# Kernel tuning notes

Measured on AMD Instinct MI355X. Metric: run time of the kernel, lower is better.

## Reference

```python
import jax, jax.numpy as jnp
import numpy as np

HIDDEN = 2048
N_HEADS = 32
N_KV_HEADS = 8
HEAD_DIM = HIDDEN // N_HEADS  # 64
N_GROUPS = N_HEADS // N_KV_HEADS  # 4
EPS = 1e-6
BATCH = 2
SEQ = 2048


def setup_inputs() -> dict:
    key = jax.random.key(0)
    ks = jax.random.split(key, 8)
    s = 1.0 / np.sqrt(HIDDEN)
    return {
        "hidden_states": jax.random.normal(ks[0], (BATCH, SEQ, HIDDEN), jnp.float32),
        # torch nn.Linear weights: [out_features, in_features]
        "Wq": jax.random.normal(ks[1], (N_HEADS * HEAD_DIM, HIDDEN), jnp.float32) * s,
        "Wk": jax.random.normal(ks[2], (N_KV_HEADS * HEAD_DIM, HIDDEN), jnp.float32) * s,
        "Wv": jax.random.normal(ks[3], (N_KV_HEADS * HEAD_DIM, HIDDEN), jnp.float32) * s,
        "Wo": jax.random.normal(ks[4], (HIDDEN, N_HEADS * HEAD_DIM), jnp.float32) * s,
        "q_norm_weight": jnp.ones((HEAD_DIM,), jnp.float32),
        "k_norm_weight": jnp.ones((HEAD_DIM,), jnp.float32),
    }


def _rmsnorm(x, w, eps=EPS):
    # x: [..., head_dim]
    rms = jax.lax.rsqrt(jnp.mean(x * x, axis=-1, keepdims=True) + eps)
    return x * rms * w


def reference(hidden_states, Wq, Wk, Wv, Wo, q_norm_weight, k_norm_weight):
    B, S, _ = hidden_states.shape
    # projections (y = x @ W.T)
    q = jnp.einsum('bsh,oh->bso', hidden_states, Wq)
    k = jnp.einsum('bsh,oh->bso', hidden_states, Wk)
    v = jnp.einsum('bsh,oh->bso', hidden_states, Wv)
    # [B, H, S, D]
    q = q.reshape(B, S, N_HEADS, HEAD_DIM).transpose(0, 2, 1, 3)
    k = k.reshape(B, S, N_KV_HEADS, HEAD_DIM).transpose(0, 2, 1, 3)
    v = v.reshape(B, S, N_KV_HEADS, HEAD_DIM).transpose(0, 2, 1, 3)
    # GQA repeat_interleave along head dim
    k = jnp.repeat(k, N_GROUPS, axis=1)
    v = jnp.repeat(v, N_GROUPS, axis=1)
    # fused QK RMSNorm
    q = _rmsnorm(q, q_norm_weight)
    k = _rmsnorm(k, k_norm_weight)
    # scaled dot-product attention with causal mask
    scale = 1.0 / np.sqrt(HEAD_DIM)
    scores = jnp.einsum('bhqd,bhkd->bhqk', q, k) * scale
    causal = jnp.tril(jnp.ones((S, S), dtype=bool))
    scores = jnp.where(causal, scores, jnp.finfo(scores.dtype).min)
    attn = jax.nn.softmax(scores, axis=-1)
    out = jnp.einsum('bhqk,bhkd->bhqd', attn, v)  # [B, H, S, D]
    out = out.transpose(0, 2, 1, 3).reshape(B, S, N_HEADS * HEAD_DIM)
    return jnp.einsum('bso,ho->bsh', out, Wo)
```

## Files before the change

### kernel.cpp

```cpp
#include <hip/hip_runtime.h>

typedef _Float16 f16;
typedef _Float16 f16x8 __attribute__((ext_vector_type(8)));
typedef _Float16 f16x4 __attribute__((ext_vector_type(4)));
typedef __fp16 fp16x2 __attribute__((ext_vector_type(2)));
typedef float f32x4 __attribute__((ext_vector_type(4)));

#define HID 2048
#define NH 32
#define NKV 8
#define HD 64
#define SEQ 2048
#define NB 2

__device__ __forceinline__ void gload_lds16(const void* g, void* l) {
  __builtin_amdgcn_global_load_lds((const __attribute__((address_space(1))) void*)g,
                                   (__attribute__((address_space(3))) void*)l, 16, 0, 0);
}

__device__ __forceinline__ uint cvt_pk_f16(float a, float b) {
  auto v = __builtin_amdgcn_cvt_pkrtz(a, b);
  uint u;
  __builtin_memcpy(&u, &v, 4);
  return u;
}

__device__ __forceinline__ float fdot2_ones(uint pk, float acc) {
  fp16x2 a;
  __builtin_memcpy(&a, &pk, 4);
  fp16x2 ones = {(__fp16)1.0f, (__fp16)1.0f};
  return __builtin_amdgcn_fdot2(a, ones, acc, false);
}

__global__ __launch_bounds__(256) void cvt_all(const float* __restrict__ X,
                                               const float* __restrict__ Wq,
                                               const float* __restrict__ Wk,
                                               const float* __restrict__ Wv,
                                               const float* __restrict__ Wo,
                                               f16* __restrict__ Xb, f16* __restrict__ Wqb,
                                               f16* __restrict__ Wkb, f16* __restrict__ Wvb,
                                               f16* __restrict__ Wob) {
  long i = (long)blockIdx.x * 256 + threadIdx.x;
  const float* s; f16* d; long o;
  if (i < 2097152)      { s = X;  d = Xb;  o = i; }
  else if (i < 3145728) { s = Wq; d = Wqb; o = i - 2097152; }
  else if (i < 3407872) { s = Wk; d = Wkb; o = i - 3145728; }
  else if (i < 3670016) { s = Wv; d = Wvb; o = i - 3407872; }
  else                  { s = Wo; d = Wob; o = i - 3670016; }
  float4 v = ((const float4*)s)[o];
  f16x4 ov = { (f16)v.x, (f16)v.y, (f16)v.z, (f16)v.w };
  ((f16x4*)d)[o] = ov;
}

template <typename CT>
__global__ __launch_bounds__(256) void gemm_bt(const f16* __restrict__ A,
                                               const f16* __restrict__ Bm,
                                               CT* __restrict__ C0, CT* __restrict__ C1,
                                               int M, int N, int K,
                                               int n_split, int ldc0, int ldc1) {
  __shared__ f16 As[2][128 * 64];
  __shared__ f16 Bs[2][128 * 64];
  const int t = threadIdx.x;
  const int lane = t & 63;
  const int w = t >> 6;
  const int wr = w >> 1, wc = w & 1;
  const int g = lane >> 4;
  const int lr = lane & 15;

  const int nwg = gridDim.x * gridDim.y;
  const int orig = blockIdx.y * gridDim.x + blockIdx.x;
  const int wg = (orig & 7) * (nwg >> 3) + (orig >> 3);
  const int m0 = (wg / gridDim.x) * 128;
  const int n0 = (wg % gridDim.x) * 128;

  f32x4 acc[4][4] = {};

  const int nkt = K / 64;

  auto stage = [&](int buf, int kt) {
    const int k0 = kt * 64;
#pragma unroll
    for (int i = 0; i < 4; ++i) {
      int c = w * 4 + i;
      int o = c * 1024 + lane * 16;
      int row = o >> 7;
      int ss = ((o >> 4) & 7) ^ (row & 7);
      const char* srcA = (const char*)A + ((size_t)(m0 + row) * K + k0) * 2 + ss * 16;
      gload_lds16(srcA, (char*)(&As[buf][0]) + c * 1024);
      const char* srcB = (const char*)Bm + ((size_t)(n0 + row) * K + k0) * 2 + ss * 16;
      gload_lds16(srcB, (char*)(&Bs[buf][0]) + c * 1024);
    }
  };

  stage(0, 0);
  if (nkt > 1) stage(1, 1);
  for (int kt = 0; kt < nkt; ++kt) {
    const int cur = kt & 1;
    if (kt + 1 < nkt) asm volatile("s_waitcnt vmcnt(8)" ::: "memory");
    else              asm volatile("s_waitcnt vmcnt(0)" ::: "memory");
    __builtin_amdgcn_s_barrier();
    __builtin_amdgcn_sched_barrier(0);

    f16x8 af[2][4], bf[2][4];
#pragma unroll
    for (int ks = 0; ks < 2; ++ks)
#pragma unroll
      for (int mf = 0; mf < 4; ++mf) {
        int row = wr * 64 + mf * 16 + lr;
        int slot = (g + 4 * ks) ^ (row & 7);
        af[ks][mf] = *(const f16x8*)((const char*)(&As[cur][0]) + row * 128 + slot * 16);
      }
#pragma unroll
    for (int ks = 0; ks < 2; ++ks)
#pragma unroll
      for (int nf = 0; nf < 4; ++nf) {
        int row = wc * 64 + nf * 16 + lr;
        int slot = (g + 4 * ks) ^ (row & 7);
        bf[ks][nf] = *(const f16x8*)((const char*)(&Bs[cur][0]) + row * 128 + slot * 16);
      }
    asm volatile("s_waitcnt lgkmcnt(0)" ::: "memory");
    __builtin_amdgcn_sched_barrier(0);
    __builtin_amdgcn_s_barrier();

    if (kt + 2 < nkt) stage(cur, kt + 2);

    __builtin_amdgcn_s_setprio(1);
#pragma unroll
    for (int ks = 0; ks < 2; ++ks)
#pragma unroll
      for (int mf = 0; mf < 4; ++mf)
#pragma unroll
        for (int nf = 0; nf < 4; ++nf)
          acc[mf][nf] = __builtin_amdgcn_mfma_f32_16x16x32_f16(af[ks][mf], bf[ks][nf], acc[mf][nf], 0, 0, 0);
    __builtin_amdgcn_s_setprio(0);
  }

  CT* Cp; int ldc, nb;
  if (n0 < n_split) { Cp = C0; ldc = ldc0; nb = n0; }
  else              { Cp = C1; ldc = ldc1; nb = n0 - n_split; }
#pragma unroll
  for (int mf = 0; mf < 4; ++mf)
#pragma unroll
    for (int nf = 0; nf < 4; ++nf)
#pragma unroll
      for (int r = 0; r < 4; ++r) {
        int mm = m0 + wr * 64 + mf * 16 + g * 4 + r;
        int nn = nb + wc * 64 + nf * 16 + lr;
        Cp[(size_t)mm * ldc + nn] = (CT)acc[mf][nf][r];
      }
}

__global__ __launch_bounds__(256) void vtrans(f16* __restrict__ KV,
                                              f16* __restrict__ VT,
                                              const float* __restrict__ kw) {
  __shared__ f16 tile[64][72];
  int t = threadIdx.x;
  int st = blockIdx.x, hk = blockIdx.y, b = blockIdx.z;

#pragma unroll
  for (int p = 0; p < 2; ++p) {
    int idx = p * 256 + t;
    int s = idx >> 3, c8 = (idx & 7) * 8;
    f16* kp = KV + (size_t)(b * SEQ + st * 64 + s) * 1024 + hk * 64 + c8;
    f16x8 kv = *(const f16x8*)kp;
    float ss = 0.f;
#pragma unroll
    for (int j = 0; j < 8; ++j) { float x = (float)kv[j]; ss += x * x; }
    ss += __shfl_xor(ss, 1); ss += __shfl_xor(ss, 2); ss += __shfl_xor(ss, 4);
    float sc = rsqrtf(ss * (1.0f / 64.0f) + 1e-6f);
    f16x8 on;
#pragma unroll
    for (int j = 0; j < 8; ++j) on[j] = (f16)((float)kv[j] * sc * kw[c8 + j]);
    *(f16x8*)kp = on;
  }

#pragma unroll
  for (int p = 0; p < 2; ++p) {
    int idx = p * 256 + t;
    int s = idx >> 3, c8 = (idx & 7) * 8;
    f16x8 v = *(const f16x8*)(KV + (size_t)(b * SEQ + st * 64 + s) * 1024 + 512 + hk * 64 + c8);
    *(f16x8*)(&tile[s][c8]) = v;
  }
  __syncthreads();
#pragma unroll
  for (int p = 0; p < 2; ++p) {
    int idx = p * 256 + t;
    int d = idx >> 3, s8 = (idx & 7) * 8;
    f16x8 ov;
#pragma unroll
    for (int j = 0; j < 8; ++j) {
      int pos = s8 + j;
      int k = (pos & 32) | (((pos >> 2) & 1) << 4) | (((pos >> 4) & 1) << 3)
            | (((pos >> 3) & 1) << 2) | (pos & 3);
      ov[j] = tile[k][d];
    }
    *(f16x8*)(VT + ((size_t)((b * NKV + hk) * 64) + d) * SEQ + st * 64 + s8) = ov;
  }
}

__global__ __launch_bounds__(512) void attn(const f16* __restrict__ Q,
                                            const f16* __restrict__ KV,
                                            const f16* __restrict__ VT,
                                            f16* __restrict__ AO,
                                            const float* __restrict__ qw) {
  __shared__ f16 Ks[3][64 * 64];
  __shared__ f16 Vs[3][64 * 64];
  const int t = threadIdx.x, lane = t & 63, w = t >> 6;
  const int g = lane >> 4, lr = lane & 15;
  const int col = blockIdx.x;
  const int qt = 31 - blockIdx.y;
  const int b = col & 1;
  const int h = 2 * (col >> 1) + (w >> 2);
  const int rg = w & 3;
  const int hk = h >> 2;
  const int q0 = qt * 64;

  const size_t qrow = (size_t)(b * SEQ + q0 + rg * 16 + lr);
  f16x8 qf[2];
  qf[0] = *(const f16x8*)(Q + qrow * HID + h * 64 + g * 8);
  qf[1] = *(const f16x8*)(Q + qrow * HID + h * 64 + g * 8 + 32);

  {
    float ss = 0.f;
#pragma unroll
    for (int i = 0; i < 2; ++i)
#pragma unroll
      for (int j = 0; j < 8; ++j) { float x = (float)qf[i][j]; ss += x * x; }
    ss += __shfl_xor(ss, 16); ss += __shfl_xor(ss, 32);
    float sc = rsqrtf(ss * (1.0f / 64.0f) + 1e-6f) * 0.125f;
    const float4* qw4 = (const float4*)qw;
    float4 w0 = qw4[2 * g], w1 = qw4[2 * g + 1];
    float4 w2 = qw4[2 * g + 8], w3 = qw4[2 * g + 9];
    qf[0][0] = (f16)((float)qf[0][0] * sc * w0.x);
    qf[0][1] = (f16)((float)qf[0][1] * sc * w0.y);
    qf[0][2] = (f16)((float)qf[0][2] * sc * w0.z);
    qf[0][3] = (f16)((float)qf[0][3] * sc * w0.w);
    qf[0][4] = (f16)((float)qf[0][4] * sc * w1.x);
    qf[0][5] = (f16)((float)qf[0][5] * sc * w1.y);
    qf[0][6] = (f16)((float)qf[0][6] * sc * w1.z);
    qf[0][7] = (f16)((float)qf[0][7] * sc * w1.w);
    qf[1][0] = (f16)((float)qf[1][0] * sc * w2.x);
    qf[1][1] = (f16)((float)qf[1][1] * sc * w2.y);
    qf[1][2] = (f16)((float)qf[1][2] * sc * w2.z);
    qf[1][3] = (f16)((float)qf[1][3] * sc * w2.w);
    qf[1][4] = (f16)((float)qf[1][4] * sc * w3.x);
    qf[1][5] = (f16)((float)qf[1][5] * sc * w3.y);
    qf[1][6] = (f16)((float)qf[1][6] * sc * w3.z);
    qf[1][7] = (f16)((float)qf[1][7] * sc * w3.w);
  }

  int koff[2][4], voff[2][4];
#pragma unroll
  for (int ks = 0; ks < 2; ++ks)
#pragma unroll
    for (int nf = 0; nf < 4; ++nf) {
      int row = nf * 16 + lr;
      koff[ks][nf] = row * 128 + (((g + 4 * ks) ^ (row & 7)) * 16);
    }
#pragma unroll
  for (int m = 0; m < 2; ++m)
#pragma unroll
    for (int df = 0; df < 4; ++df) {
      int row = df * 16 + lr;
      voff[m][df] = row * 128 + (((4 * m + g) ^ (row & 7)) * 16);
    }

  f32x4 oacc[4] = {};
  float psum0 = 0.0f, psum1 = 0.0f;

  const int nkt = qt + 1;

  auto stage = [&](int buf, int kt2) {
    int o = w * 1024 + lane * 16;
    int row = o >> 7;
    int ss = ((o >> 4) & 7) ^ (row & 7);
    gload_lds16((const char*)KV + ((size_t)(b * SEQ + kt2 * 64 + row) * 1024 + hk * 64) * 2 + ss * 16,
                (char*)(&Ks[buf][0]) + w * 1024);
    gload_lds16((const char*)VT + (((size_t)((b * NKV + hk) * 64) + row) * SEQ + kt2 * 64) * 2 + ss * 16,
                (char*)(&Vs[buf][0]) + w * 1024);
  };

  stage(0, 0);
  if (nkt > 1) stage(1, 1);
  int cur = 0;
  for (int kt = 0; kt < nkt; ++kt) {
    if (kt + 1 < nkt) asm volatile("s_waitcnt vmcnt(2)" ::: "memory");
    else              asm volatile("s_waitcnt vmcnt(0)" ::: "memory");
    __builtin_amdgcn_s_barrier();
    asm volatile("" ::: "memory");

    if (kt + 2 < nkt) {
      int nb = cur + 2; if (nb >= 3) nb -= 3;
      stage(nb, kt + 2);
    }

    const char* Kb = (const char*)(&Ks[cur][0]);
    const char* Vb = (const char*)(&Vs[cur][0]);

    f32x4 sacc[4] = {};
#pragma unroll
    for (int ks = 0; ks < 2; ++ks) {
      __builtin_amdgcn_s_setprio(1);
#pragma unroll
      for (int nf = 0; nf < 4; ++nf) {
        f16x8 kf = *(const f16x8*)(Kb + koff[ks][nf]);
        sacc[nf] = __builtin_amdgcn_mfma_f32_16x16x32_f16(kf, qf[ks], sacc[nf], 0, 0, 0);
      }
      __builtin_amdgcn_s_setprio(0);
    }

    if (kt == qt) {
      int qq = q0 + rg * 16 + lr;
#pragma unroll
      for (int nf = 0; nf < 4; ++nf) {
        int kvb = kt * 64 + nf * 16 + g * 4;
#pragma unroll
        for (int r = 0; r < 4; ++r)
          if (kvb + r > qq) sacc[nf][r] = -1e30f;
      }
    }

    uint pk[8];
#pragma unroll
    for (int nf = 0; nf < 4; ++nf) {
      float p0 = __expf(sacc[nf][0]);
      float p1 = __expf(sacc[nf][1]);
      float p2 = __expf(sacc[nf][2]);
      float p3 = __expf(sacc[nf][3]);
      pk[2 * nf]     = cvt_pk_f16(p0, p1);
      pk[2 * nf + 1] = cvt_pk_f16(p2, p3);
      psum0 = fdot2_ones(pk[2 * nf], psum0);
      psum1 = fdot2_ones(pk[2 * nf + 1], psum1);
    }

#pragma unroll
    for (int m = 0; m < 2; ++m) {
      union { uint u[4]; f16x8 v; } pu;
      pu.u[0] = pk[4 * m];     pu.u[1] = pk[4 * m + 1];
      pu.u[2] = pk[4 * m + 2]; pu.u[3] = pk[4 * m + 3];
      __builtin_amdgcn_s_setprio(1);
#pragma unroll
      for (int df = 0; df < 4; ++df) {
        f16x8 vf = *(const f16x8*)(Vb + voff[m][df]);
        oacc[df] = __builtin_amdgcn_mfma_f32_16x16x32_f16(pu.v, vf, oacc[df], 0, 0, 0);
      }
      __builtin_amdgcn_s_setprio(0);
    }

    cur = (cur == 2) ? 0 : cur + 1;
  }

  float psum = psum0 + psum1;
  psum += __shfl_xor(psum, 16);
  psum += __shfl_xor(psum, 32);
  float pdiv[4];
#pragma unroll
  for (int r = 0; r < 4; ++r) pdiv[r] = __shfl(psum, g * 4 + r);

#pragma unroll
  for (int df = 0; df < 4; ++df)
#pragma unroll
    for (int r = 0; r < 4; ++r) {
      size_t rowg = (size_t)(b * SEQ + q0 + rg * 16 + g * 4 + r);
      AO[rowg * HID + h * 64 + df * 16 + lr] = (f16)(oacc[df][r] / pdiv[r]);
    }
}

extern "C" void kernel_launch(void* const* d_in, const int* in_sizes, int n_in,
                              void* d_out, int out_size, void* d_ws, size_t ws_size,
                              hipStream_t stream) {
  const float* X  = (const float*)d_in[0];
  const float* Wq = (const float*)d_in[1];
  const float* Wk = (const float*)d_in[2];
  const float* Wv = (const float*)d_in[3];
  const float* Wo = (const float*)d_in[4];
  const float* qw = (const float*)d_in[5];
  const float* kw = (const float*)d_in[6];

  char* ws = (char*)d_ws;
  f16* Xb   = (f16*)(ws + 0);
  f16* Wqkv = (f16*)(ws + 16777216);
  f16* Wob  = (f16*)(ws + 29360128);
  f16* Qb   = (f16*)(ws + 37748736);
  f16* KVb  = (f16*)(ws + 54525952);
  f16* VTb  = (f16*)(ws + 62914560);
  f16* AOb  = (f16*)(ws + 67108864);
  float* OUT = (float*)d_out;

  cvt_all<<<18432, 256, 0, stream>>>(X, Wq, Wk, Wv, Wo,
                                     Xb, Wqkv, Wqkv + 2048 * 2048, Wqkv + 2560 * 2048, Wob);

  gemm_bt<f16><<<dim3(24, 32), 256, 0, stream>>>(Xb, Wqkv, Qb, KVb,
                                                 4096, 3072, 2048, 2048, 2048, 1024);

  vtrans<<<dim3(32, 8, 2), 256, 0, stream>>>(KVb, VTb, kw);
  attn<<<dim3(32, 32, 1), 512, 0, stream>>>(Qb, KVb, VTb, AOb, qw);

  gemm_bt<float><<<dim3(16, 32), 256, 0, stream>>>(AOb, Wob, OUT, OUT,
                                                   4096, 2048, 2048, 2048, 2048, 2048);
}
```

Baseline: 169.3 us.

## Use 256x256-tile QKV GEMM and exp2-based softmax with reciprocal normalization

Adds a new 512-thread GEMM kernel with 256x256 output tiles and uses it for the QKV projection instead of the 128x128 kernel. Each wave now holds 8x4 MFMA accumulators, which raises data reuse per LDS load but lowers the grid to 192 blocks and uses 128KB of LDS. In attention, log2(e) is folded into the Q scale so exp2f replaces __expf, and the final divide becomes a reciprocal multiply. The larger tile adds register pressure and may under-fill the CUs.

```diff
diff --git a/kernel.cpp b/kernel.cpp
--- a/kernel.cpp
+++ b/kernel.cpp
@@ -52,6 +52,103 @@
   ((f16x4*)d)[o] = ov;
 }
 
+__global__ __launch_bounds__(512) void gemm_bt256(const f16* __restrict__ A,
+                                                  const f16* __restrict__ Bm,
+                                                  f16* __restrict__ C0, f16* __restrict__ C1,
+                                                  int M, int N, int K,
+                                                  int n_split, int ldc0, int ldc1) {
+  __shared__ f16 As[2][256 * 64];
+  __shared__ f16 Bs[2][256 * 64];
+  const int t = threadIdx.x;
+  const int lane = t & 63;
+  const int w = t >> 6;
+  const int wr = w >> 2, wc = w & 3;
+  const int g = lane >> 4;
+  const int lr = lane & 15;
+
+  const int nwg = gridDim.x * gridDim.y;
+  const int orig = blockIdx.y * gridDim.x + blockIdx.x;
+  const int wg = (orig & 7) * (nwg >> 3) + (orig >> 3);
+  const int m0 = (wg / gridDim.x) * 256;
+  const int n0 = (wg % gridDim.x) * 256;
+
+  f32x4 acc[8][4] = {};
+
+  const int nkt = K / 64;
+
+  auto stage = [&](int buf, int kt) {
+    const int k0 = kt * 64;
+#pragma unroll
+    for (int i = 0; i < 4; ++i) {
+      int c = w * 4 + i;
+      int o = c * 1024 + lane * 16;
+      int row = o >> 7;
+      int ss = ((o >> 4) & 7) ^ (row & 7);
+      const char* srcA = (const char*)A + ((size_t)(m0 + row) * K + k0) * 2 + ss * 16;
+      gload_lds16(srcA, (char*)(&As[buf][0]) + c * 1024);
+      const char* srcB = (const char*)Bm + ((size_t)(n0 + row) * K + k0) * 2 + ss * 16;
+      gload_lds16(srcB, (char*)(&Bs[buf][0]) + c * 1024);
+    }
+  };
+
+  stage(0, 0);
+  stage(1, 1);
+  for (int kt = 0; kt < nkt; ++kt) {
+    const int cur = kt & 1;
+    if (kt + 1 < nkt) asm volatile("s_waitcnt vmcnt(8)" ::: "memory");
+    else              asm volatile("s_waitcnt vmcnt(0)" ::: "memory");
+    __builtin_amdgcn_s_barrier();
+    __builtin_amdgcn_sched_barrier(0);
+
+    f16x8 af[2][8], bf[2][4];
+#pragma unroll
+    for (int ks = 0; ks < 2; ++ks)
+#pragma unroll
+      for (int mf = 0; mf < 8; ++mf) {
+        int row = wr * 128 + mf * 16 + lr;
+        int slot = (g + 4 * ks) ^ (row & 7);
+        af[ks][mf] = *(const f16x8*)((const char*)(&As[cur][0]) + row * 128 + slot * 16);
+      }
+#pragma unroll
+    for (int ks = 0; ks < 2; ++ks)
+#pragma unroll
+      for (int nf = 0; nf < 4; ++nf) {
+        int row = wc * 64 + nf * 16 + lr;
+        int slot = (g + 4 * ks) ^ (row & 7);
+        bf[ks][nf] = *(const f16x8*)((const char*)(&Bs[cur][0]) + row * 128 + slot * 16);
+      }
+    asm volatile("s_waitcnt lgkmcnt(0)" ::: "memory");
+    __builtin_amdgcn_sched_barrier(0);
+    __builtin_amdgcn_s_barrier();
+
+    if (kt + 2 < nkt) stage(cur, kt + 2);
+
+    __builtin_amdgcn_s_setprio(1);
+#pragma unroll
+    for (int ks = 0; ks < 2; ++ks)
+#pragma unroll
+      for (int mf = 0; mf < 8; ++mf)
+#pragma unroll
+        for (int nf = 0; nf < 4; ++nf)
+          acc[mf][nf] = __builtin_amdgcn_mfma_f32_16x16x32_f16(af[ks][mf], bf[ks][nf], acc[mf][nf], 0, 0, 0);
+    __builtin_amdgcn_s_setprio(0);
+  }
+
+  f16* Cp; int ldc, nb;
+  if (n0 < n_split) { Cp = C0; ldc = ldc0; nb = n0; }
+  else              { Cp = C1; ldc = ldc1; nb = n0 - n_split; }
+#pragma unroll
+  for (int mf = 0; mf < 8; ++mf)
+#pragma unroll
+    for (int nf = 0; nf < 4; ++nf)
+#pragma unroll
+      for (int r = 0; r < 4; ++r) {
+        int mm = m0 + wr * 128 + mf * 16 + g * 4 + r;
+        int nn = nb + wc * 64 + nf * 16 + lr;
+        Cp[(size_t)mm * ldc + nn] = (f16)acc[mf][nf][r];
+      }
+}
+
 template <typename CT>
 __global__ __launch_bounds__(256) void gemm_bt(const f16* __restrict__ A,
                                                const f16* __restrict__ Bm,
@@ -227,7 +324,7 @@
 #pragma unroll
       for (int j = 0; j < 8; ++j) { float x = (float)qf[i][j]; ss += x * x; }
     ss += __shfl_xor(ss, 16); ss += __shfl_xor(ss, 32);
-    float sc = rsqrtf(ss * (1.0f / 64.0f) + 1e-6f) * 0.125f;
+    float sc = rsqrtf(ss * (1.0f / 64.0f) + 1e-6f) * (0.125f * 1.44269504f);
     const float4* qw4 = (const float4*)qw;
     float4 w0 = qw4[2 * g], w1 = qw4[2 * g + 1];
     float4 w2 = qw4[2 * g + 8], w3 = qw4[2 * g + 9];
@@ -323,10 +420,10 @@
     uint pk[8];
 #pragma unroll
     for (int nf = 0; nf < 4; ++nf) {
-      float p0 = __expf(sacc[nf][0]);
-      float p1 = __expf(sacc[nf][1]);
-      float p2 = __expf(sacc[nf][2]);
-      float p3 = __expf(sacc[nf][3]);
+      float p0 = exp2f(sacc[nf][0]);
+      float p1 = exp2f(sacc[nf][1]);
+      float p2 = exp2f(sacc[nf][2]);
+      float p3 = exp2f(sacc[nf][3]);
       pk[2 * nf]     = cvt_pk_f16(p0, p1);
       pk[2 * nf + 1] = cvt_pk_f16(p2, p3);
       psum0 = fdot2_ones(pk[2 * nf], psum0);
@@ -355,14 +452,14 @@
   psum += __shfl_xor(psum, 32);
   float pdiv[4];
 #pragma unroll
-  for (int r = 0; r < 4; ++r) pdiv[r] = __shfl(psum, g * 4 + r);
+  for (int r = 0; r < 4; ++r) pdiv[r] = 1.0f / __shfl(psum, g * 4 + r);
 
 #pragma unroll
   for (int df = 0; df < 4; ++df)
 #pragma unroll
     for (int r = 0; r < 4; ++r) {
       size_t rowg = (size_t)(b * SEQ + q0 + rg * 16 + g * 4 + r);
-      AO[rowg * HID + h * 64 + df * 16 + lr] = (f16)(oacc[df][r] / pdiv[r]);
+      AO[rowg * HID + h * 64 + df * 16 + lr] = (f16)(oacc[df][r] * pdiv[r]);
     }
 }
 
@@ -390,8 +487,8 @@
   cvt_all<<<18432, 256, 0, stream>>>(X, Wq, Wk, Wv, Wo,
                                      Xb, Wqkv, Wqkv + 2048 * 2048, Wqkv + 2560 * 2048, Wob);
 
-  gemm_bt<f16><<<dim3(24, 32), 256, 0, stream>>>(Xb, Wqkv, Qb, KVb,
-                                                 4096, 3072, 2048, 2048, 2048, 1024);
+  gemm_bt256<<<dim3(12, 16), 512, 0, stream>>>(Xb, Wqkv, Qb, KVb,
+                                               4096, 3072, 2048, 2048, 2048, 1024);
 
   vtrans<<<dim3(32, 8, 2), 256, 0, stream>>>(KVb, VTb, kw);
   attn<<<dim3(32, 32, 1), 512, 0, stream>>>(Qb, KVb, VTb, AOb, qw);
```

New measurement: 220.4 us. 1.3x slower.
